# Kernel optimization log

Measured on AMD Instinct MI355X. Metric: run time of the kernel, lower is better.

The kernel has to match this reference:

```python
import math
import jax, jax.numpy as jnp
import numpy as np

V, D, E, NH, HD, L, FF, RH = 32000, 512, 4, 8, 64, 2, 2048, 256
MPL, MV = 3, 2  # max_path_len, max_visits_per_expert


def _ln(x):
    m = x.mean(-1, keepdims=True)
    v = ((x - m) ** 2).mean(-1, keepdims=True)
    return (x - m) / jnp.sqrt(v + 1e-5)


def _pe(S, d):
    pos = np.arange(S, dtype=np.float32)[:, None]
    div = np.exp(np.arange(0, d, 2, dtype=np.float32) * (-math.log(10000.0) / d))
    pe = np.zeros((S, d), np.float32)
    pe[:, 0::2] = np.sin(pos * div)
    pe[:, 1::2] = np.cos(pos * div)
    return jnp.asarray(pe)[None]  # [1,S,D]


def setup_inputs() -> dict:
    key = jax.random.key(0)
    ks = jax.random.split(key, 24)
    n = lambda k, shp, s=0.02: (jax.random.normal(k, shp, jnp.float32) * s)
    input_ids = jax.random.randint(ks[0], (8, 256), 0, V, dtype=jnp.int32)
    emb = n(ks[1], (V, D)).at[0].set(0.0)  # padding_idx=0
    return {
        "input_ids": input_ids,
        "emb": emb,
        "r_w1": n(ks[2], (RH, D)), "r_b1": jnp.zeros((RH,), jnp.float32),
        "r_w2": n(ks[3], (E + 1, RH)), "r_b2": jnp.zeros((E + 1,), jnp.float32),
        "r_q": jnp.zeros((E + 1,), jnp.float32),
        "in_w": n(ks[4], (E, L, 3 * D, D)), "in_b": jnp.zeros((E, L, 3 * D), jnp.float32),
        "out_w": n(ks[5], (E, L, D, D)), "out_b": jnp.zeros((E, L, D), jnp.float32),
        "gate_w": n(ks[6], (E, L, D, 2 * D)), "gate_b": jnp.zeros((E, L, D), jnp.float32),
        "f_w1": n(ks[7], (E, L, FF, D)), "f_b1": jnp.zeros((E, L, FF), jnp.float32),
        "f_w2": n(ks[8], (E, L, D, FF)), "f_b2": jnp.zeros((E, L, D), jnp.float32),
        "tag": n(ks[9], (E, 1, 1, D), 0.01),
        "lm_w": n(ks[10], (V, D)), "lm_b": jnp.zeros((V,), jnp.float32),
    }


def reference(input_ids, emb, r_w1, r_b1, r_w2, r_b2, r_q,
              in_w, in_b, out_w, out_b, gate_w, gate_b,
              f_w1, f_b1, f_w2, f_b2, tag, lm_w, lm_b):
    B, S = input_ids.shape

    def mha(h, w, b, ow, ob):
        qkv = h @ w.T + b  # [B,S,3D]
        q, k, v = jnp.split(qkv, 3, axis=-1)
        q = q.reshape(B, S, NH, HD); k = k.reshape(B, S, NH, HD); v = v.reshape(B, S, NH, HD)
        att = jax.nn.softmax(jnp.einsum('bqhd,bkhd->bhqk', q, k) / math.sqrt(HD), axis=-1)
        o = jnp.einsum('bhqk,bkhd->bqhd', att, v).reshape(B, S, D)
        return o @ ow.T + ob

    def expert_fwd(p, h):
        iw, ib, ow, ob, gw, gb, w1, b1, w2, b2, tg = p
        for l in range(L):
            z = _ln(h)  # norm1
            ao = mha(z, iw[l], ib[l], ow[l], ob[l])
            g = jax.nn.sigmoid(jnp.concatenate([z, ao], -1) @ gw[l].T + gb[l])
            h = h + _ln(z + g * ao)  # GatedAttention norm + residual
            z2 = _ln(h)  # norm2
            h = h + jax.nn.gelu(z2 @ w1[l].T + b1[l], approximate=False) @ w2[l].T + b2[l]
        return h + tg

    x = emb[input_ids] * math.sqrt(D)
    x = _ln(x + _pe(S, D))  # pos_encoder + input_norm (dropout=eval identity)

    visits = jnp.zeros((B, E), jnp.int32)
    active = jnp.ones((B,), bool)
    ep = (in_w, in_b, out_w, out_b, gate_w, gate_b, f_w1, f_b1, f_w2, f_b2, tag)

    for _ in range(MPL):
        summary = x.mean(axis=1)  # [B,D]
        logits = jax.nn.gelu(summary @ r_w1.T + r_b1, approximate=False) @ r_w2.T + r_b2
        fl = jnp.clip(_ln(logits + r_q[None, :]), -10.0, 10.0)
        ext = jnp.concatenate([visits >= MV, jnp.zeros((B, 1), bool)], axis=-1)
        fl = jnp.where(ext, -jnp.inf, fl)
        action = jnp.argmax(fl, axis=-1)  # E == terminate
        do = active & (action < E)
        all_out = jax.vmap(expert_fwd, in_axes=(0, None))(ep, x)  # [E,B,S,D]
        sel = jax.nn.one_hot(jnp.where(do, action, 0), E, dtype=x.dtype) * do[:, None].astype(x.dtype)
        nx = jnp.einsum('ebsd,be->bsd', all_out, sel)
        x = jnp.where(do[:, None, None], nx, x)
        visits = visits + (sel > 0).astype(jnp.int32)
        active = do

    return _ln(x) @ lm_w.T + lm_b  # final_norm + lm_head  [B,S,V]
```

## Files before the change

### kernel.cpp

```cpp
#include <hip/hip_runtime.h>
#include <hip/hip_bf16.h>
#include <math.h>

#define BB   8
#define SS   256
#define DD   512
#define NHH  8
#define HDD  64
#define EE   4
#define LL   2
#define FFF  2048
#define RHH  256
#define VV   32000
#define MVV  2
#define TOK  (BB*SS)
#define CASTBLK 44672

typedef __attribute__((ext_vector_type(8))) short bf16x8;
typedef __attribute__((ext_vector_type(4))) float f32x4;

__device__ __forceinline__ float wred_sum(float v){
#pragma unroll
  for(int o=32;o;o>>=1) v += __shfl_xor(v,o,64);
  return v;
}
__device__ __forceinline__ float block_sum(float v, float* sh){
  v = wred_sum(v);
  if((threadIdx.x&63)==0) sh[threadIdx.x>>6]=v;
  __syncthreads();
  float t = sh[0]+sh[1]+sh[2]+sh[3];
  __syncthreads();
  return t;
}
__device__ __forceinline__ float gelu_exact(float x){
  return 0.5f*x*(1.f+erff(x*0.70710678118654752f));
}
__device__ __forceinline__ unsigned short bfr(float f){
  union{float f; unsigned u;} c; c.f=f;
  unsigned u = c.u;
  return (unsigned short)((u + 0x7FFFu + ((u>>16)&1u)) >> 16);
}
__device__ __forceinline__ float bff(unsigned short u){
  union{unsigned u; float f;} c; c.u = ((unsigned)u)<<16; return c.f;
}

__global__ void k_preproc(const float* __restrict__ s0,const float* __restrict__ s1,
                          const float* __restrict__ s2,const float* __restrict__ s3,
                          const float* __restrict__ s4,const float* __restrict__ s5,
                          unsigned short* __restrict__ d0,unsigned short* __restrict__ d1,
                          unsigned short* __restrict__ d2,unsigned short* __restrict__ d3,
                          unsigned short* __restrict__ d4,unsigned short* __restrict__ d5,
                          const int* __restrict__ ids, const float* __restrict__ emb,
                          float* __restrict__ x){
  __shared__ float sh[4];
  if(blockIdx.x < CASTBLK){
    long i = (long)blockIdx.x*256 + threadIdx.x;
    const float* s; unsigned short* d; long o;
    if(i < 1572864L){ s=s0; d=d0; o=i; }
    else if(i < 2097152L){ s=s1; d=d1; o=i-1572864L; }
    else if(i < 3145728L){ s=s2; d=d2; o=i-2097152L; }
    else if(i < 5242880L){ s=s3; d=d3; o=i-3145728L; }
    else if(i < 7340032L){ s=s4; d=d4; o=i-5242880L; }
    else { s=s5; d=d5; o=i-7340032L; }
    float4 v = ((const float4*)s)[o];
    ushort4 u; u.x=bfr(v.x); u.y=bfr(v.y); u.z=bfr(v.z); u.w=bfr(v.w);
    ((ushort4*)d)[o] = u;
    return;
  }
  int tok = blockIdx.x - CASTBLK;
  int s = tok & (SS-1);
  int tid = threadIdx.x;
  int id = ids[tok];
  float v[2];
#pragma unroll
  for(int i=0;i<2;i++){
    int d = tid + i*256;
    float e = emb[(size_t)id*DD + d] * 22.627416997969522f;
    int j = d >> 1;
    float freq = expf((float)(2*j) * (-0.0179889460390160f));
    float arg = (float)s * freq;
    v[i] = e + ((d & 1) ? cosf(arg) : sinf(arg));
  }
  float m = block_sum(v[0]+v[1], sh) * (1.f/DD);
  float dd0=v[0]-m, dd1=v[1]-m;
  float var = block_sum(dd0*dd0+dd1*dd1, sh) * (1.f/DD);
  float inv = rsqrtf(var + 1e-5f);
  float* q = x + (size_t)tok*DD;
  q[tid] = dd0*inv; q[tid+256] = dd1*inv;
}

__global__ __launch_bounds__(256)
void k_compose(const unsigned short* __restrict__ out_wb, const float* __restrict__ out_b,
               const unsigned short* __restrict__ gate_wb,
               unsigned short* __restrict__ wext, float* __restrict__ cb){
  int combo = blockIdx.x;
  const unsigned short* Wa2 = gate_wb + (size_t)combo*DD*2*DD + 512;
  const unsigned short* Wo  = out_wb  + (size_t)combo*DD*DD;
  int c0 = blockIdx.y*64;
  int t = threadIdx.x;
  if(blockIdx.z == 4){
    const float* ob = out_b + (size_t)combo*DD;
    int c = c0 + (t>>2), q = t&3;
    float s = 0.f;
    for(int j=q*128; j<q*128+128; j++) s += bff(Wa2[(size_t)c*1024 + j]) * ob[j];
    s += __shfl_xor(s,1,64);
    s += __shfl_xor(s,2,64);
    if(q==0) cb[(size_t)combo*DD + c] = s;
    return;
  }
  int kb = blockIdx.z*128;
  __shared__ unsigned short sA[64*64];
  __shared__ unsigned short sWT[128*64];
  int lane = t & 63, w = t >> 6;
  int wcol0 = w*32;
  f32x4 acc[4][2];
#pragma unroll
  for(int m=0;m<4;m++)
#pragma unroll
    for(int n=0;n<2;n++) acc[m][n] = (f32x4){0.f,0.f,0.f,0.f};

  for(int j0 = 0; j0 < DD; j0 += 64){
    {
      int sr = t>>3, ss8 = t&7;
#pragma unroll
      for(int i=0;i<2;i++){
        int r = i*32 + sr;
        int ce = ((ss8<<4) ^ ((r&7)<<4)) >> 1;
        const unsigned short* gp = Wa2 + (size_t)(c0+r)*1024 + j0 + ce;
        __builtin_amdgcn_global_load_lds((const __attribute__((address_space(1))) void*)gp,
            (__attribute__((address_space(3))) void*)(sA + i*2048 + t*8), 16, 0, 0);
      }
    }
    {
      int jr = t>>2, cg = (t&3)*32;
      const unsigned short* gp = Wo + (size_t)(j0+jr)*DD + kb + cg;
      bf16x8 v0 = *(const bf16x8*)gp;
      bf16x8 v1 = *(const bf16x8*)(gp+8);
      bf16x8 v2 = *(const bf16x8*)(gp+16);
      bf16x8 v3 = *(const bf16x8*)(gp+24);
#pragma unroll
      for(int e=0;e<8;e++){
        int n0 = cg+e;
        *(unsigned short*)((char*)sWT + n0*128      + ((jr*2) ^ ((n0&7)<<4)))     = (unsigned short)v0[e];
        int n1 = cg+8+e;
        *(unsigned short*)((char*)sWT + n1*128      + ((jr*2) ^ ((n1&7)<<4)))     = (unsigned short)v1[e];
        int n2 = cg+16+e;
        *(unsigned short*)((char*)sWT + n2*128      + ((jr*2) ^ ((n2&7)<<4)))     = (unsigned short)v2[e];
        int n3 = cg+24+e;
        *(unsigned short*)((char*)sWT + n3*128      + ((jr*2) ^ ((n3&7)<<4)))     = (unsigned short)v3[e];
      }
    }
    asm volatile("s_waitcnt vmcnt(0)" ::: "memory");
    __syncthreads();
#pragma unroll
    for(int ks=0; ks<2; ks++){
      bf16x8 af[4], wf[2];
#pragma unroll
      for(int m=0;m<4;m++){
        int r = m*16 + (lane & 15);
        af[m] = *(const bf16x8*)((const char*)sA + r*128 + (((((lane>>4)<<4)|(ks<<6))) ^ ((r&7)<<4)));
      }
#pragma unroll
      for(int n=0;n<2;n++){
        int r = wcol0 + n*16 + (lane & 15);
        wf[n] = *(const bf16x8*)((const char*)sWT + r*128 + (((((lane>>4)<<4)|(ks<<6))) ^ ((r&7)<<4)));
      }
#pragma unroll
      for(int m=0;m<4;m++)
#pragma unroll
        for(int n=0;n<2;n++)
          acc[m][n] = __builtin_amdgcn_mfma_f32_16x16x32_bf16(af[m], wf[n], acc[m][n], 0, 0, 0);
    }
    __syncthreads();
  }
  int orow0 = c0 + ((lane >> 4) << 2);
  int ocol0 = kb + wcol0 + (lane & 15);
#pragma unroll
  for(int m=0;m<4;m++)
#pragma unroll
    for(int n=0;n<2;n++){
      int col = ocol0 + n*16;
#pragma unroll
      for(int j=0;j<4;j++){
        int row = orow0 + m*16 + j;
        wext[(size_t)combo*DD*DD + (size_t)row*DD + col] = bfr(acc[m][n][j]);
      }
    }
}

__global__ void k_lnpsum(const float* __restrict__ xin, const float* __restrict__ P0,
                         const float* __restrict__ P1, float* __restrict__ xout,
                         unsigned short* __restrict__ zb,
                         float* __restrict__ psum, const int* __restrict__ dof){
  __shared__ float sh[4];
  int tid = threadIdx.x;
  if(blockIdx.x < TOK){
    int tok = blockIdx.x; int b = tok>>8;
    size_t base = (size_t)tok*DD;
    float a0 = xin[base+tid], a1 = xin[base+tid+256];
    if(P0){
      if(dof[b]){
        a0 += P0[base+tid]     + P1[base+tid];
        a1 += P0[base+tid+256] + P1[base+tid+256];
      }
      xout[base+tid] = a0; xout[base+tid+256] = a1;
    }
    float m = block_sum(a0+a1, sh) * (1.f/DD);
    float d0=a0-m, d1=a1-m;
    float var = block_sum(d0*d0+d1*d1, sh) * (1.f/DD);
    float inv = rsqrtf(var + 1e-5f);
    zb[base+tid] = bfr(d0*inv); zb[base+tid+256] = bfr(d1*inv);
  } else {
    int pb = blockIdx.x - TOK; int b = pb>>4, p = pb&15;
    bool c = (P0 != nullptr) && dof[b];
    float s0=0.f, s1=0.f;
    for(int tt=0; tt<16; tt++){
      size_t r = (size_t)(b*SS + p*16 + tt)*DD;
      float v0 = xin[r+tid], v1 = xin[r+tid+256];
      if(c){ v0 += P0[r+tid]+P1[r+tid]; v1 += P0[r+tid+256]+P1[r+tid+256]; }
      s0 += v0; s1 += v1;
    }
    float* q = psum + (size_t)(b*16+p)*DD;
    q[tid] = s0; q[tid+256] = s1;
  }
}

__global__ void k_router(const float* __restrict__ psum,
                         const float* __restrict__ r_w1, const float* __restrict__ r_b1,
                         const float* __restrict__ r_w2, const float* __restrict__ r_b2,
                         const float* __restrict__ r_q,
                         int* __restrict__ action, int* __restrict__ dof,
                         int* __restrict__ visits, int* __restrict__ active, int step){
  int b = blockIdx.x; int tid = threadIdx.x;
  if(step==0 && tid==0){ active[b]=1; for(int e=0;e<EE;e++) visits[b*EE+e]=0; }
  __shared__ float ssum[DD];
  __shared__ float hid[RHH];
  __shared__ float lg[EE+1];
  float s0=0.f, s1=0.f;
  for(int p=0;p<16;p++){
    const float* q = psum + (size_t)(b*16+p)*DD;
    s0 += q[tid]; s1 += q[tid+256];
  }
  ssum[tid] = s0*(1.f/SS); ssum[tid+256] = s1*(1.f/SS);
  __syncthreads();
  float acc = r_b1[tid];
  const float4* wr4 = (const float4*)(r_w1 + (size_t)tid*DD);
  for(int d4=0; d4<DD/4; d4++){
    float4 wv = wr4[d4];
    float4 sv = *(const float4*)&ssum[d4*4];
    acc += wv.x*sv.x + wv.y*sv.y + wv.z*sv.z + wv.w*sv.w;
  }
  hid[tid] = gelu_exact(acc);
  __syncthreads();
  if(tid < EE+1){
    const float* w2 = r_w2 + (size_t)tid*RHH;
    float a = r_b2[tid] + r_q[tid];
    for(int j=0;j<RHH;j++) a += hid[j]*w2[j];
    lg[tid]=a;
  }
  __syncthreads();
  if(tid==0){
    float m=0.f; for(int k=0;k<EE+1;k++) m+=lg[k]; m *= (1.f/(EE+1));
    float v=0.f; for(int k=0;k<EE+1;k++){float d=lg[k]-m; v+=d*d;} v *= (1.f/(EE+1));
    float inv = rsqrtf(v+1e-5f);
    float best=-1e38f; int bi=0;
    for(int k=0;k<EE+1;k++){
      float fl = (lg[k]-m)*inv;
      fl = fminf(fmaxf(fl,-10.f),10.f);
      if(k<EE && visits[b*EE+k]>=MVV) fl = -1e38f;
      if(fl > best){best=fl; bi=k;}
    }
    int dd = (active[b] && bi<EE) ? 1 : 0;
    action[b]=bi; dof[b]=dd;
    if(dd) visits[b*EE+bi]++;
    active[b]=dd;
  }
}

template<int EPI>
__device__ __forceinline__ void mg64(
    unsigned short* sA, unsigned short* sW,
    const unsigned short* __restrict__ A, int Ald,
    const unsigned short* __restrict__ W, int Wld,
    const float* __restrict__ bias, const float* __restrict__ tagv,
    int N, int K,
    float* __restrict__ Cf, unsigned short* __restrict__ Cb,
    int rowbase, int colbase){
  int t = threadIdx.x;
  int lane = t & 63;
  int w = t >> 6;
  int wcol0 = w*32;
  int sr = t >> 3, ss8 = t & 7;

  f32x4 acc[4][2];
#pragma unroll
  for(int m=0;m<4;m++)
#pragma unroll
    for(int n=0;n<2;n++) acc[m][n] = (f32x4){0.f,0.f,0.f,0.f};

  auto STAGE = [&](int buf, int k0){
    unsigned short* dA = sA + buf*4096;
    unsigned short* dW = sW + buf*8192;
#pragma unroll
    for(int i = 0; i < 2; i++){
      int r  = i*32 + sr;
      int ce = ((ss8<<4) ^ ((r&7)<<4)) >> 1;
      const unsigned short* gp = A + (size_t)(rowbase + r)*Ald + k0 + ce;
      __builtin_amdgcn_global_load_lds((const __attribute__((address_space(1))) void*)gp,
          (__attribute__((address_space(3))) void*)(dA + i*2048 + t*8), 16, 0, 0);
    }
#pragma unroll
    for(int i = 0; i < 4; i++){
      int r  = i*32 + sr;
      int ce = ((ss8<<4) ^ ((r&7)<<4)) >> 1;
      const unsigned short* gw = W + (size_t)(colbase + r)*Wld + k0 + ce;
      __builtin_amdgcn_global_load_lds((const __attribute__((address_space(1))) void*)gw,
          (__attribute__((address_space(3))) void*)(dW + i*2048 + t*8), 16, 0, 0);
    }
  };

  STAGE(0, 0);
  int cur = 0;
  for(int k0 = 0; k0 < K; k0 += 64){
    if(k0 + 64 < K){
      STAGE(cur^1, k0+64);
      asm volatile("s_waitcnt vmcnt(6)" ::: "memory");
    } else {
      asm volatile("s_waitcnt vmcnt(0)" ::: "memory");
    }
    __builtin_amdgcn_s_barrier();
    __builtin_amdgcn_sched_barrier(0);
    const char* bA = (const char*)(sA + cur*4096);
    const char* bW = (const char*)(sW + cur*8192);
#pragma unroll
    for(int ks = 0; ks < 2; ks++){
      bf16x8 af[4], wf[2];
#pragma unroll
      for(int m = 0; m < 4; m++){
        int r = m*16 + (lane & 15);
        af[m] = *(const bf16x8*)(bA + r*128 + (((((lane>>4)<<4)|(ks<<6))) ^ ((r&7)<<4)));
      }
#pragma unroll
      for(int n = 0; n < 2; n++){
        int r = wcol0 + n*16 + (lane & 15);
        wf[n] = *(const bf16x8*)(bW + r*128 + (((((lane>>4)<<4)|(ks<<6))) ^ ((r&7)<<4)));
      }
#pragma unroll
      for(int m = 0; m < 4; m++)
#pragma unroll
        for(int n = 0; n < 2; n++)
          acc[m][n] = __builtin_amdgcn_mfma_f32_16x16x32_bf16(af[m], wf[n], acc[m][n], 0, 0, 0);
    }
    asm volatile("s_waitcnt lgkmcnt(0)" ::: "memory");
    __builtin_amdgcn_s_barrier();
    cur ^= 1;
  }
  int orow0 = rowbase + ((lane >> 4) << 2);
  int ocol0 = colbase + wcol0 + (lane & 15);
#pragma unroll
  for(int m = 0; m < 4; m++){
#pragma unroll
    for(int n = 0; n < 2; n++){
      int col = ocol0 + n*16;
      float addv = (bias ? bias[col] : 0.f) + (tagv ? tagv[col] : 0.f);
#pragma unroll
      for(int j = 0; j < 4; j++){
        int row = orow0 + m*16 + j;
        size_t idx = (size_t)row*N + col;
        float v = acc[m][n][j] + addv;
        if(EPI == 0){ if(Cf) Cf[idx] = v; if(Cb) Cb[idx] = bfr(v); }
        else if(EPI == 1){ Cb[idx] = bfr(gelu_exact(v)); }
        else { Cf[idx] += v; }
      }
    }
  }
}

#define GEMM_LDS __shared__ unsigned short sA[2*64*64]; __shared__ unsigned short sW[2*128*64];

__global__ __launch_bounds__(256)
void k_qkvgate(const unsigned short* __restrict__ z_bf,
               const unsigned short* __restrict__ in_wb, const float* __restrict__ in_b,
               const unsigned short* __restrict__ gate_wb, const float* __restrict__ gate_b,
               unsigned short* __restrict__ qkv_bf, float* __restrict__ gtmp, int l,
               const int* __restrict__ action, const int* __restrict__ dof){
  GEMM_LDS
  int b = blockIdx.x; if(!dof[b]) return;
  size_t o = (size_t)(action[b]*LL + l);
  int rowbase = b*SS + blockIdx.y*64;
  int zz = blockIdx.z;
  if(zz < 12){
    mg64<0>(sA,sW, z_bf,DD, in_wb + o*3*DD*DD, DD, in_b + o*3*DD, nullptr,
            3*DD, DD, nullptr, qkv_bf, rowbase, zz*128);
  } else {
    mg64<0>(sA,sW, z_bf,DD, gate_wb + o*DD*2*DD, 2*DD, gate_b + o*DD, nullptr,
            DD, DD, gtmp, nullptr, rowbase, (zz-12)*128);
  }
}

__global__ __launch_bounds__(256)
void k_outgate(const unsigned short* __restrict__ attno_bf,
               const unsigned short* __restrict__ out_wb, const float* __restrict__ out_b,
               const unsigned short* __restrict__ wext, const float* __restrict__ cb,
               unsigned short* __restrict__ ao_bf, float* __restrict__ gtmp, int l,
               const int* __restrict__ action, const int* __restrict__ dof){
  GEMM_LDS
  int b = blockIdx.x; if(!dof[b]) return;
  size_t o = (size_t)(action[b]*LL + l);
  int rowbase = b*SS + blockIdx.y*64;
  int zz = blockIdx.z;
  if(zz < 4){
    mg64<0>(sA,sW, attno_bf,DD, out_wb + o*DD*DD, DD, out_b + o*DD, nullptr,
            DD, DD, nullptr, ao_bf, rowbase, zz*128);
  } else {
    mg64<2>(sA,sW, attno_bf,DD, wext + o*DD*DD, DD, cb + o*DD, nullptr,
            DD, DD, gtmp, nullptr, rowbase, (zz-4)*128);
  }
}

__global__ __launch_bounds__(256)
void k_ffn1(const unsigned short* __restrict__ z2_bf,
            const unsigned short* __restrict__ f_w1b, const float* __restrict__ f_b1,
            unsigned short* __restrict__ ffh_bf, int l,
            const int* __restrict__ action, const int* __restrict__ dof){
  GEMM_LDS
  int b = blockIdx.x; if(!dof[b]) return;
  size_t o = (size_t)(action[b]*LL + l);
  mg64<1>(sA,sW, z2_bf,DD, f_w1b + o*FFF*DD, DD, f_b1 + o*FFF, nullptr,
          FFF, DD, nullptr, ffh_bf, b*SS + blockIdx.y*64, blockIdx.z*128);
}

__global__ __launch_bounds__(256)
void k_ffn2(const unsigned short* __restrict__ ffh_bf,
            const unsigned short* __restrict__ f_w2b, const float* __restrict__ f_b2,
            const float* __restrict__ tag,
            float* __restrict__ P0, float* __restrict__ P1, int l,
            const int* __restrict__ action, const int* __restrict__ dof){
  GEMM_LDS
  int b = blockIdx.x; if(!dof[b]) return;
  size_t o = (size_t)(action[b]*LL + l);
  int half = blockIdx.z >> 2, colb = (blockIdx.z & 3)*128;
  const float* bias = half ? nullptr : (f_b2 + o*DD);
  const float* tagv = (half==0 && l==LL-1) ? (tag + (size_t)action[b]*DD) : nullptr;
  mg64<0>(sA,sW, ffh_bf + half*1024, FFF, f_w2b + o*DD*FFF + half*1024, FFF,
          bias, tagv, DD, 1024, half ? P1 : P0, nullptr,
          b*SS + blockIdx.y*64, colb);
}

__global__ __launch_bounds__(256)
void k_attn(const unsigned short* __restrict__ qkv, unsigned short* __restrict__ attno,
            const int* __restrict__ dof){
  int bh = blockIdx.x; int b = bh>>3, h = bh&7;
  if(!dof[b]) return;
  int q0 = blockIdx.y*64;
  __shared__ unsigned short sK[256*64];
  __shared__ unsigned short sVT[64*256];
  int t = threadIdx.x, l = t&63, w = t>>6;
  const unsigned short* qbase = qkv + (size_t)b*SS*1536;

  {
    int sr = t>>3, s8 = t&7;
#pragma unroll
    for(int i=0;i<8;i++){
      int r = i*32 + sr;
      int ce = ((s8<<4) ^ ((r&7)<<4)) >> 1;
      const unsigned short* gp = qbase + (size_t)r*1536 + 512 + h*64 + ce;
      __builtin_amdgcn_global_load_lds((const __attribute__((address_space(1))) void*)gp,
          (__attribute__((address_space(3))) void*)(sK + i*2048 + t*8), 16, 0, 0);
    }
  }
  {
    int kt0 = t>>2, dg = (t&3)*16;
#pragma unroll
    for(int i=0;i<4;i++){
      int kt = i*64 + kt0;
      const unsigned short* gp = qbase + (size_t)kt*1536 + 1024 + h*64 + dg;
      bf16x8 v0 = *(const bf16x8*)gp;
      bf16x8 v1 = *(const bf16x8*)(gp+8);
#pragma unroll
      for(int e=0;e<8;e++){
        int d  = dg+e;
        *(unsigned short*)((char*)sVT + d*512  + ((kt*2) ^ ((d&7)<<4)))  = (unsigned short)v0[e];
        int d2 = dg+8+e;
        *(unsigned short*)((char*)sVT + d2*512 + ((kt*2) ^ ((d2&7)<<4))) = (unsigned short)v1[e];
      }
    }
  }
  bf16x8 qf[2];
  {
    const unsigned short* qrow = qbase + (size_t)(q0 + w*16 + (l&15))*1536 + h*64;
    qf[0] = *(const bf16x8*)(qrow + ((l>>4)<<3));
    qf[1] = *(const bf16x8*)(qrow + ((l>>4)<<3) + 32);
  }
  __syncthreads();

  f32x4 sacc[16];
#pragma unroll
  for(int kb=0;kb<16;kb++) sacc[kb] = (f32x4){0.f,0.f,0.f,0.f};
#pragma unroll
  for(int kb=0;kb<16;kb++){
    int rk = kb*16 + (l&15);
#pragma unroll
    for(int ks=0;ks<2;ks++){
      bf16x8 kf = *(const bf16x8*)((const char*)sK + rk*128 + (((((l>>4)<<4)|(ks<<6))) ^ ((rk&7)<<4)));
      sacc[kb] = __builtin_amdgcn_mfma_f32_16x16x32_bf16(qf[ks], kf, sacc[kb], 0, 0, 0);
    }
  }
  float rden[4];
#pragma unroll
  for(int j=0;j<4;j++){
    float m = -1e38f;
#pragma unroll
    for(int kb=0;kb<16;kb++) m = fmaxf(m, sacc[kb][j]);
#pragma unroll
    for(int o=1;o<16;o<<=1) m = fmaxf(m, __shfl_xor(m,o,64));
    m *= 0.125f;
    float s = 0.f;
#pragma unroll
    for(int kb=0;kb<16;kb++){
      float e = expf(sacc[kb][j]*0.125f - m);
      sacc[kb][j] = e; s += e;
    }
#pragma unroll
    for(int o=1;o<16;o<<=1) s += __shfl_xor(s,o,64);
    rden[j] = 1.f/s;
  }
  __syncthreads();

  char* sP = (char*)sK + w*8192;
#pragma unroll
  for(int kb=0;kb<16;kb++){
    int k = kb*16 + (l&15);
#pragma unroll
    for(int j=0;j<4;j++){
      int qr = ((l>>4)<<2) + j;
      *(unsigned short*)(sP + qr*512 + ((k*2) ^ ((qr&7)<<4))) = bfr(sacc[kb][j]);
    }
  }
  __syncthreads();

  f32x4 oacc[4];
#pragma unroll
  for(int df=0;df<4;df++) oacc[df] = (f32x4){0.f,0.f,0.f,0.f};
#pragma unroll
  for(int kstep=0;kstep<8;kstep++){
    bf16x8 pa = *(const bf16x8*)(sP + (l&15)*512 + ((((kstep<<6)|((l>>4)<<4))) ^ ((l&7)<<4)));
#pragma unroll
    for(int df=0;df<4;df++){
      int d = df*16 + (l&15);
      bf16x8 vb = *(const bf16x8*)((char*)sVT + d*512 + ((((kstep<<6)|((l>>4)<<4))) ^ ((d&7)<<4)));
      oacc[df] = __builtin_amdgcn_mfma_f32_16x16x32_bf16(pa, vb, oacc[df], 0, 0, 0);
    }
  }
  int orow0 = b*SS + q0 + w*16 + ((l>>4)<<2);
#pragma unroll
  for(int df=0;df<4;df++){
    int col = h*64 + df*16 + (l&15);
#pragma unroll
    for(int j=0;j<4;j++)
      attno[(size_t)(orow0+j)*DD + col] = bfr(oacc[df][j]*rden[j]);
  }
}

__global__ void k_gateres_ln(const unsigned short* __restrict__ zb,
                             const unsigned short* __restrict__ aob,
                             const float* __restrict__ g, float* __restrict__ x,
                             unsigned short* __restrict__ z2b, const int* __restrict__ dof){
  int tok = blockIdx.x; if(!dof[tok>>8]) return;
  __shared__ float sh[4];
  int tid=threadIdx.x;
  size_t base=(size_t)tok*DD;
  float zz0=bff(zb[base+tid]),     aa0=bff(aob[base+tid]),     gg0=g[base+tid];
  float zz1=bff(zb[base+tid+256]), aa1=bff(aob[base+tid+256]), gg1=g[base+tid+256];
  float t0 = zz0 + aa0/(1.f+expf(-gg0));
  float t1 = zz1 + aa1/(1.f+expf(-gg1));
  float m = block_sum(t0+t1,sh)*(1.f/DD);
  float d0=t0-m, d1=t1-m;
  float var=block_sum(d0*d0+d1*d1,sh)*(1.f/DD);
  float inv=rsqrtf(var+1e-5f);
  float xn0 = x[base+tid]     + d0*inv;
  float xn1 = x[base+tid+256] + d1*inv;
  x[base+tid] = xn0; x[base+tid+256] = xn1;
  float m2 = block_sum(xn0+xn1,sh)*(1.f/DD);
  float e0=xn0-m2, e1=xn1-m2;
  float var2=block_sum(e0*e0+e1*e1,sh)*(1.f/DD);
  float inv2=rsqrtf(var2+1e-5f);
  z2b[base+tid] = bfr(e0*inv2); z2b[base+tid+256] = bfr(e1*inv2);
}

__global__ __launch_bounds__(512)
void k_lmgemm(const unsigned short* __restrict__ A, const unsigned short* __restrict__ W,
              const float* __restrict__ bias, float* __restrict__ C){
  __shared__ unsigned short sA[2*256*64];
  __shared__ unsigned short sW[2*256*64];
  int t = threadIdx.x, lane = t & 63, w = t >> 6;
  int wr = w >> 2, wc = w & 3;
  int rowbase = blockIdx.y*256, colbase = blockIdx.z*256;
  int sr = t >> 3, ss8 = t & 7;

  f32x4 acc[8][4];
#pragma unroll
  for(int m=0;m<8;m++)
#pragma unroll
    for(int n=0;n<4;n++) acc[m][n] = (f32x4){0.f,0.f,0.f,0.f};

  auto STAGE = [&](int buf, int k0){
    unsigned short* dA = sA + buf*16384;
    unsigned short* dW = sW + buf*16384;
#pragma unroll
    for(int i = 0; i < 4; i++){
      int r  = i*64 + sr;
      int ce = ((ss8<<4) ^ ((r&7)<<4)) >> 1;
      const unsigned short* gp = A + (size_t)(rowbase + r)*DD + k0 + ce;
      __builtin_amdgcn_global_load_lds((const __attribute__((address_space(1))) void*)gp,
          (__attribute__((address_space(3))) void*)(dA + i*4096 + t*8), 16, 0, 0);
      const unsigned short* gw = W + (size_t)(colbase + r)*DD + k0 + ce;
      __builtin_amdgcn_global_load_lds((const __attribute__((address_space(1))) void*)gw,
          (__attribute__((address_space(3))) void*)(dW + i*4096 + t*8), 16, 0, 0);
    }
  };

  STAGE(0, 0);
  int cur = 0;
  for(int k0 = 0; k0 < DD; k0 += 64){
    if(k0 + 64 < DD){
      STAGE(cur^1, k0+64);
      asm volatile("s_waitcnt vmcnt(8)" ::: "memory");
    } else {
      asm volatile("s_waitcnt vmcnt(0)" ::: "memory");
    }
    __builtin_amdgcn_s_barrier();
    __builtin_amdgcn_sched_barrier(0);
    const char* bA = (const char*)(sA + cur*16384);
    const char* bW = (const char*)(sW + cur*16384);
#pragma unroll
    for(int ks = 0; ks < 2; ks++){
      bf16x8 af[8], wf[4];
#pragma unroll
      for(int m = 0; m < 8; m++){
        int r = wr*128 + m*16 + (lane & 15);
        af[m] = *(const bf16x8*)(bA + r*128 + (((((lane>>4)<<4)|(ks<<6))) ^ ((r&7)<<4)));
      }
#pragma unroll
      for(int n = 0; n < 4; n++){
        int r = wc*64 + n*16 + (lane & 15);
        wf[n] = *(const bf16x8*)(bW + r*128 + (((((lane>>4)<<4)|(ks<<6))) ^ ((r&7)<<4)));
      }
#pragma unroll
      for(int m = 0; m < 8; m++)
#pragma unroll
        for(int n = 0; n < 4; n++)
          acc[m][n] = __builtin_amdgcn_mfma_f32_16x16x32_bf16(af[m], wf[n], acc[m][n], 0, 0, 0);
    }
    asm volatile("s_waitcnt lgkmcnt(0)" ::: "memory");
    __builtin_amdgcn_s_barrier();
    cur ^= 1;
  }
  int orow0 = rowbase + wr*128 + ((lane >> 4) << 2);
  int ocol0 = colbase + wc*64 + (lane & 15);
#pragma unroll
  for(int m = 0; m < 8; m++){
#pragma unroll
    for(int n = 0; n < 4; n++){
      int col = ocol0 + n*16;
      float bv = bias[col];
#pragma unroll
      for(int j = 0; j < 4; j++){
        int row = orow0 + m*16 + j;
        C[(size_t)row*VV + col] = acc[m][n][j] + bv;
      }
    }
  }
}

extern "C" void kernel_launch(void* const* d_in, const int* in_sizes, int n_in,
                              void* d_out, int out_size, void* d_ws, size_t ws_size,
                              hipStream_t stream){
  const int*   ids   = (const int*)d_in[0];
  const float* emb   = (const float*)d_in[1];
  const float* r_w1  = (const float*)d_in[2];
  const float* r_b1  = (const float*)d_in[3];
  const float* r_w2  = (const float*)d_in[4];
  const float* r_b2  = (const float*)d_in[5];
  const float* r_q   = (const float*)d_in[6];
  const float* in_w  = (const float*)d_in[7];
  const float* in_b  = (const float*)d_in[8];
  const float* out_w = (const float*)d_in[9];
  const float* out_b = (const float*)d_in[10];
  const float* gate_w= (const float*)d_in[11];
  const float* gate_b= (const float*)d_in[12];
  const float* f_w1  = (const float*)d_in[13];
  const float* f_b1  = (const float*)d_in[14];
  const float* f_w2  = (const float*)d_in[15];
  const float* f_b2  = (const float*)d_in[16];
  const float* tag   = (const float*)d_in[17];
  const float* lm_w  = (const float*)d_in[18];
  const float* lm_b  = (const float*)d_in[19];
  float* out = (float*)d_out;
  float* ws  = (float*)d_ws;

  const size_t M = (size_t)TOK*DD;
  float* x0     = ws;
  float* x1     = ws + 1*M;
  float* gtmp   = ws + 2*M;
  float* P0     = ws + 3*M;
  float* P1     = ws + 4*M;
  float* psum   = ws + 5*M;
  float* cbias  = ws + 5*M + 65536;
  int*   ipool  = (int*)(ws + 5*M + 65536 + 4096);
  int* action = ipool; int* dof = ipool+BB; int* active = ipool+2*BB; int* visits = ipool+3*BB;

  unsigned short* ub = (unsigned short*)(ws + 5*M + 65536 + 4096 + 64);
  unsigned short* z_bf     = ub;
  unsigned short* z2_bf    = ub + 1*M;
  unsigned short* attno_bf = ub + 2*M;
  unsigned short* ao_bf    = ub + 3*M;
  unsigned short* qkv_bf   = ub + 4*M;
  unsigned short* ffh_bf   = ub + 7*M;
  unsigned short* wb = ub + 11*M;
  unsigned short* in_wb   = wb;
  unsigned short* out_wb  = in_wb  + (size_t)EE*LL*3*DD*DD;
  unsigned short* gate_wb = out_wb + (size_t)EE*LL*DD*DD;
  unsigned short* f_w1b   = gate_wb+ (size_t)EE*LL*DD*2*DD;
  unsigned short* f_w2b   = f_w1b  + (size_t)EE*LL*FFF*DD;
  unsigned short* lm_wb   = f_w2b  + (size_t)EE*LL*DD*FFF;
  unsigned short* wext_b  = lm_wb  + (size_t)VV*DD;

  k_preproc<<<CASTBLK+TOK,256,0,stream>>>(in_w,out_w,gate_w,f_w1,f_w2,lm_w,
                                          in_wb,out_wb,gate_wb,f_w1b,f_w2b,lm_wb,
                                          ids, emb, x0);
  k_compose<<<dim3(8,8,5),256,0,stream>>>(out_wb, out_b, gate_wb, wext_b, cbias);

  float* xc = x0;
  for(int step=0; step<3; step++){
    float* xn = (xc==x0) ? x1 : x0;
    if(step==0)
      k_lnpsum<<<TOK+128,256,0,stream>>>(xc, nullptr, nullptr, xn, z_bf, psum, dof);
    else{
      k_lnpsum<<<TOK+128,256,0,stream>>>(xc, P0, P1, xn, z_bf, psum, dof);
      xc = xn;
    }
    k_router<<<BB,256,0,stream>>>(psum,r_w1,r_b1,r_w2,r_b2,r_q,action,dof,visits,active,step);
    for(int l=0; l<LL; l++){
      if(l==1){
        float* xn2 = (xc==x0) ? x1 : x0;
        k_lnpsum<<<TOK,256,0,stream>>>(xc, P0, P1, xn2, z_bf, nullptr, dof);
        xc = xn2;
      }
      k_qkvgate<<<dim3(BB,4,16),256,0,stream>>>(z_bf, in_wb,in_b, gate_wb,gate_b,
                                                qkv_bf, gtmp, l, action, dof);
      k_attn<<<dim3(BB*NHH,4),256,0,stream>>>(qkv_bf, attno_bf, dof);
      k_outgate<<<dim3(BB,4,8),256,0,stream>>>(attno_bf, out_wb,out_b, wext_b,cbias,
                                               ao_bf, gtmp, l, action, dof);
      k_gateres_ln<<<TOK,256,0,stream>>>(z_bf, ao_bf, gtmp, xc, z2_bf, dof);
      k_ffn1<<<dim3(BB,4,16),256,0,stream>>>(z2_bf, f_w1b,f_b1, ffh_bf, l, action, dof);
      k_ffn2<<<dim3(BB,4,8),256,0,stream>>>(ffh_bf, f_w2b,f_b2, tag, P0, P1, l, action, dof);
    }
  }

  {
    float* xn = (xc==x0) ? x1 : x0;
    k_lnpsum<<<TOK,256,0,stream>>>(xc, P0, P1, xn, z_bf, nullptr, dof);
  }
  k_lmgemm<<<dim3(1,8,VV/256),512,0,stream>>>(z_bf, lm_wb, lm_b, out);
}
```

Measured before the change: 730.7 us.

## Fuse per-layer kernels into one persistent kernel with grid barriers

Replaces the six per-layer launches (qkv/gate GEMM, attention, out/gate GEMM, gated residual LN, FFN1, FFN2) with a single 256-block persistent kernel. The stages are separated by a software grid-wide barrier built on atomics, and work units are mapped onto fixed blocks. This removes kernel launch gaps and idle tails between small stages. The cost is reduced parallelism for the stages that previously used 512 blocks, a 64KB static LDS allocation that may limit occupancy, and reliance on all 256 blocks being co-resident for the spin barrier to avoid deadlock.

```diff
diff --git a/kernel.cpp b/kernel.cpp
--- a/kernel.cpp
+++ b/kernel.cpp
@@ -44,6 +44,24 @@
   union{unsigned u; float f;} c; c.u = ((unsigned)u)<<16; return c.f;
 }
 
+__device__ __forceinline__ void gsync(unsigned* cnt, unsigned* gen){
+  __syncthreads();
+  if(threadIdx.x==0){
+    __threadfence();
+    unsigned g = __hip_atomic_load(gen, __ATOMIC_RELAXED, __HIP_MEMORY_SCOPE_AGENT);
+    unsigned a = __hip_atomic_fetch_add(cnt, 1u, __ATOMIC_ACQ_REL, __HIP_MEMORY_SCOPE_AGENT);
+    if(a == 255u){
+      __hip_atomic_store(cnt, 0u, __ATOMIC_RELAXED, __HIP_MEMORY_SCOPE_AGENT);
+      __hip_atomic_store(gen, g+1u, __ATOMIC_RELEASE, __HIP_MEMORY_SCOPE_AGENT);
+    } else {
+      while(__hip_atomic_load(gen, __ATOMIC_RELAXED, __HIP_MEMORY_SCOPE_AGENT) == g)
+        __builtin_amdgcn_s_sleep(4);
+    }
+    __threadfence();
+  }
+  __syncthreads();
+}
+
 __global__ void k_preproc(const float* __restrict__ s0,const float* __restrict__ s1,
                           const float* __restrict__ s2,const float* __restrict__ s3,
                           const float* __restrict__ s4,const float* __restrict__ s5,
@@ -51,8 +69,9 @@
                           unsigned short* __restrict__ d2,unsigned short* __restrict__ d3,
                           unsigned short* __restrict__ d4,unsigned short* __restrict__ d5,
                           const int* __restrict__ ids, const float* __restrict__ emb,
-                          float* __restrict__ x){
+                          float* __restrict__ x, unsigned* bcnt, unsigned* bgen){
   __shared__ float sh[4];
+  if(blockIdx.x==0 && threadIdx.x==0){ *bcnt = 0u; *bgen = 0u; }
   if(blockIdx.x < CASTBLK){
     long i = (long)blockIdx.x*256 + threadIdx.x;
     const float* s; unsigned short* d; long o;
@@ -141,13 +160,13 @@
 #pragma unroll
       for(int e=0;e<8;e++){
         int n0 = cg+e;
-        *(unsigned short*)((char*)sWT + n0*128      + ((jr*2) ^ ((n0&7)<<4)))     = (unsigned short)v0[e];
+        *(unsigned short*)((char*)sWT + n0*128 + ((jr*2) ^ ((n0&7)<<4))) = (unsigned short)v0[e];
         int n1 = cg+8+e;
-        *(unsigned short*)((char*)sWT + n1*128      + ((jr*2) ^ ((n1&7)<<4)))     = (unsigned short)v1[e];
+        *(unsigned short*)((char*)sWT + n1*128 + ((jr*2) ^ ((n1&7)<<4))) = (unsigned short)v1[e];
         int n2 = cg+16+e;
-        *(unsigned short*)((char*)sWT + n2*128      + ((jr*2) ^ ((n2&7)<<4)))     = (unsigned short)v2[e];
+        *(unsigned short*)((char*)sWT + n2*128 + ((jr*2) ^ ((n2&7)<<4))) = (unsigned short)v2[e];
         int n3 = cg+24+e;
-        *(unsigned short*)((char*)sWT + n3*128      + ((jr*2) ^ ((n3&7)<<4)))     = (unsigned short)v3[e];
+        *(unsigned short*)((char*)sWT + n3*128 + ((jr*2) ^ ((n3&7)<<4))) = (unsigned short)v3[e];
       }
     }
     asm volatile("s_waitcnt vmcnt(0)" ::: "memory");
@@ -376,86 +395,70 @@
   }
 }
 
-#define GEMM_LDS __shared__ unsigned short sA[2*64*64]; __shared__ unsigned short sW[2*128*64];
-
-__global__ __launch_bounds__(256)
-void k_qkvgate(const unsigned short* __restrict__ z_bf,
-               const unsigned short* __restrict__ in_wb, const float* __restrict__ in_b,
-               const unsigned short* __restrict__ gate_wb, const float* __restrict__ gate_b,
-               unsigned short* __restrict__ qkv_bf, float* __restrict__ gtmp, int l,
-               const int* __restrict__ action, const int* __restrict__ dof){
-  GEMM_LDS
-  int b = blockIdx.x; if(!dof[b]) return;
+__device__ __forceinline__ void qkvgate_unit(char* smem, const unsigned short* z_bf,
+    const unsigned short* in_wb, const float* in_b,
+    const unsigned short* gate_wb, const float* gate_b,
+    unsigned short* qkv_bf, float* gtmp, int l, const int* action,
+    int b, int y, int z){
+  unsigned short* sA = (unsigned short*)smem;
+  unsigned short* sW = (unsigned short*)(smem + 16384);
   size_t o = (size_t)(action[b]*LL + l);
-  int rowbase = b*SS + blockIdx.y*64;
-  int zz = blockIdx.z;
-  if(zz < 12){
+  int rowbase = b*SS + y*64;
+  if(z < 12)
     mg64<0>(sA,sW, z_bf,DD, in_wb + o*3*DD*DD, DD, in_b + o*3*DD, nullptr,
-            3*DD, DD, nullptr, qkv_bf, rowbase, zz*128);
-  } else {
+            3*DD, DD, nullptr, qkv_bf, rowbase, z*128);
+  else
     mg64<0>(sA,sW, z_bf,DD, gate_wb + o*DD*2*DD, 2*DD, gate_b + o*DD, nullptr,
-            DD, DD, gtmp, nullptr, rowbase, (zz-12)*128);
-  }
-}
-
-__global__ __launch_bounds__(256)
-void k_outgate(const unsigned short* __restrict__ attno_bf,
-               const unsigned short* __restrict__ out_wb, const float* __restrict__ out_b,
-               const unsigned short* __restrict__ wext, const float* __restrict__ cb,
-               unsigned short* __restrict__ ao_bf, float* __restrict__ gtmp, int l,
-               const int* __restrict__ action, const int* __restrict__ dof){
-  GEMM_LDS
-  int b = blockIdx.x; if(!dof[b]) return;
+            DD, DD, gtmp, nullptr, rowbase, (z-12)*128);
+}
+
+__device__ __forceinline__ void outgate_unit(char* smem, const unsigned short* attno_bf,
+    const unsigned short* out_wb, const float* out_b,
+    const unsigned short* wext, const float* cb,
+    unsigned short* ao_bf, float* gtmp, int l, const int* action,
+    int b, int y, int z){
+  unsigned short* sA = (unsigned short*)smem;
+  unsigned short* sW = (unsigned short*)(smem + 16384);
   size_t o = (size_t)(action[b]*LL + l);
-  int rowbase = b*SS + blockIdx.y*64;
-  int zz = blockIdx.z;
-  if(zz < 4){
+  int rowbase = b*SS + y*64;
+  if(z < 4)
     mg64<0>(sA,sW, attno_bf,DD, out_wb + o*DD*DD, DD, out_b + o*DD, nullptr,
-            DD, DD, nullptr, ao_bf, rowbase, zz*128);
-  } else {
+            DD, DD, nullptr, ao_bf, rowbase, z*128);
+  else
     mg64<2>(sA,sW, attno_bf,DD, wext + o*DD*DD, DD, cb + o*DD, nullptr,
-            DD, DD, gtmp, nullptr, rowbase, (zz-4)*128);
-  }
-}
-
-__global__ __launch_bounds__(256)
-void k_ffn1(const unsigned short* __restrict__ z2_bf,
-            const unsigned short* __restrict__ f_w1b, const float* __restrict__ f_b1,
-            unsigned short* __restrict__ ffh_bf, int l,
-            const int* __restrict__ action, const int* __restrict__ dof){
-  GEMM_LDS
-  int b = blockIdx.x; if(!dof[b]) return;
+            DD, DD, gtmp, nullptr, rowbase, (z-4)*128);
+}
+
+__device__ __forceinline__ void ffn1_unit(char* smem, const unsigned short* z2_bf,
+    const unsigned short* f_w1b, const float* f_b1,
+    unsigned short* ffh_bf, int l, const int* action, int b, int y, int z){
+  unsigned short* sA = (unsigned short*)smem;
+  unsigned short* sW = (unsigned short*)(smem + 16384);
   size_t o = (size_t)(action[b]*LL + l);
   mg64<1>(sA,sW, z2_bf,DD, f_w1b + o*FFF*DD, DD, f_b1 + o*FFF, nullptr,
-          FFF, DD, nullptr, ffh_bf, b*SS + blockIdx.y*64, blockIdx.z*128);
-}
-
-__global__ __launch_bounds__(256)
-void k_ffn2(const unsigned short* __restrict__ ffh_bf,
-            const unsigned short* __restrict__ f_w2b, const float* __restrict__ f_b2,
-            const float* __restrict__ tag,
-            float* __restrict__ P0, float* __restrict__ P1, int l,
-            const int* __restrict__ action, const int* __restrict__ dof){
-  GEMM_LDS
-  int b = blockIdx.x; if(!dof[b]) return;
+          FFF, DD, nullptr, ffh_bf, b*SS + y*64, z*128);
+}
+
+__device__ __forceinline__ void ffn2_unit(char* smem, const unsigned short* ffh_bf,
+    const unsigned short* f_w2b, const float* f_b2, const float* tag,
+    float* P0, float* P1, int l, const int* action, int b, int y, int z){
+  unsigned short* sA = (unsigned short*)smem;
+  unsigned short* sW = (unsigned short*)(smem + 16384);
   size_t o = (size_t)(action[b]*LL + l);
-  int half = blockIdx.z >> 2, colb = (blockIdx.z & 3)*128;
+  int half = z >> 2, colb = (z & 3)*128;
   const float* bias = half ? nullptr : (f_b2 + o*DD);
   const float* tagv = (half==0 && l==LL-1) ? (tag + (size_t)action[b]*DD) : nullptr;
   mg64<0>(sA,sW, ffh_bf + half*1024, FFF, f_w2b + o*DD*FFF + half*1024, FFF,
           bias, tagv, DD, 1024, half ? P1 : P0, nullptr,
-          b*SS + blockIdx.y*64, colb);
-}
-
-__global__ __launch_bounds__(256)
-void k_attn(const unsigned short* __restrict__ qkv, unsigned short* __restrict__ attno,
-            const int* __restrict__ dof){
-  int bh = blockIdx.x; int b = bh>>3, h = bh&7;
-  if(!dof[b]) return;
-  int q0 = blockIdx.y*64;
-  __shared__ unsigned short sK[256*64];
-  __shared__ unsigned short sVT[64*256];
-  int t = threadIdx.x, l = t&63, w = t>>6;
+          b*SS + y*64, colb);
+}
+
+__device__ __forceinline__ void attn_unit(char* smem,
+    const unsigned short* __restrict__ qkv, unsigned short* __restrict__ attno,
+    int b, int h, int q0){
+  unsigned short* sK  = (unsigned short*)smem;
+  unsigned short* sVT = (unsigned short*)(smem + 32768);
+  int t = threadIdx.x, ln = t&63, w = t>>6;
   const unsigned short* qbase = qkv + (size_t)b*SS*1536;
 
   {
@@ -488,9 +491,9 @@
   }
   bf16x8 qf[2];
   {
-    const unsigned short* qrow = qbase + (size_t)(q0 + w*16 + (l&15))*1536 + h*64;
-    qf[0] = *(const bf16x8*)(qrow + ((l>>4)<<3));
-    qf[1] = *(const bf16x8*)(qrow + ((l>>4)<<3) + 32);
+    const unsigned short* qrow = qbase + (size_t)(q0 + w*16 + (ln&15))*1536 + h*64;
+    qf[0] = *(const bf16x8*)(qrow + ((ln>>4)<<3));
+    qf[1] = *(const bf16x8*)(qrow + ((ln>>4)<<3) + 32);
   }
   __syncthreads();
 
@@ -499,10 +502,10 @@
   for(int kb=0;kb<16;kb++) sacc[kb] = (f32x4){0.f,0.f,0.f,0.f};
 #pragma unroll
   for(int kb=0;kb<16;kb++){
-    int rk = kb*16 + (l&15);
+    int rk = kb*16 + (ln&15);
 #pragma unroll
     for(int ks=0;ks<2;ks++){
-      bf16x8 kf = *(const bf16x8*)((const char*)sK + rk*128 + (((((l>>4)<<4)|(ks<<6))) ^ ((rk&7)<<4)));
+      bf16x8 kf = *(const bf16x8*)((const char*)sK + rk*128 + (((((ln>>4)<<4)|(ks<<6))) ^ ((rk&7)<<4)));
       sacc[kb] = __builtin_amdgcn_mfma_f32_16x16x32_bf16(qf[ks], kf, sacc[kb], 0, 0, 0);
     }
   }
@@ -530,10 +533,10 @@
   char* sP = (char*)sK + w*8192;
 #pragma unroll
   for(int kb=0;kb<16;kb++){
-    int k = kb*16 + (l&15);
+    int k = kb*16 + (ln&15);
 #pragma unroll
     for(int j=0;j<4;j++){
-      int qr = ((l>>4)<<2) + j;
+      int qr = ((ln>>4)<<2) + j;
       *(unsigned short*)(sP + qr*512 + ((k*2) ^ ((qr&7)<<4))) = bfr(sacc[kb][j]);
     }
   }
@@ -544,30 +547,29 @@
   for(int df=0;df<4;df++) oacc[df] = (f32x4){0.f,0.f,0.f,0.f};
 #pragma unroll
   for(int kstep=0;kstep<8;kstep++){
-    bf16x8 pa = *(const bf16x8*)(sP + (l&15)*512 + ((((kstep<<6)|((l>>4)<<4))) ^ ((l&7)<<4)));
+    bf16x8 pa = *(const bf16x8*)(sP + (ln&15)*512 + ((((kstep<<6)|((ln>>4)<<4))) ^ ((ln&7)<<4)));
 #pragma unroll
     for(int df=0;df<4;df++){
-      int d = df*16 + (l&15);
-      bf16x8 vb = *(const bf16x8*)((char*)sVT + d*512 + ((((kstep<<6)|((l>>4)<<4))) ^ ((d&7)<<4)));
+      int d = df*16 + (ln&15);
+      bf16x8 vb = *(const bf16x8*)((char*)sVT + d*512 + ((((kstep<<6)|((ln>>4)<<4))) ^ ((d&7)<<4)));
       oacc[df] = __builtin_amdgcn_mfma_f32_16x16x32_bf16(pa, vb, oacc[df], 0, 0, 0);
     }
   }
-  int orow0 = b*SS + q0 + w*16 + ((l>>4)<<2);
+  int orow0 = b*SS + q0 + w*16 + ((ln>>4)<<2);
 #pragma unroll
   for(int df=0;df<4;df++){
-    int col = h*64 + df*16 + (l&15);
+    int col = h*64 + df*16 + (ln&15);
 #pragma unroll
     for(int j=0;j<4;j++)
       attno[(size_t)(orow0+j)*DD + col] = bfr(oacc[df][j]*rden[j]);
   }
 }
 
-__global__ void k_gateres_ln(const unsigned short* __restrict__ zb,
-                             const unsigned short* __restrict__ aob,
-                             const float* __restrict__ g, float* __restrict__ x,
-                             unsigned short* __restrict__ z2b, const int* __restrict__ dof){
-  int tok = blockIdx.x; if(!dof[tok>>8]) return;
-  __shared__ float sh[4];
+__device__ __forceinline__ void gateres_unit(char* smem,
+    const unsigned short* __restrict__ zb, const unsigned short* __restrict__ aob,
+    const float* __restrict__ g, float* __restrict__ x,
+    unsigned short* __restrict__ z2b, int tok){
+  float* sh = (float*)smem;
   int tid=threadIdx.x;
   size_t base=(size_t)tok*DD;
   float zz0=bff(zb[base+tid]),     aa0=bff(aob[base+tid]),     gg0=g[base+tid];
@@ -586,6 +588,64 @@
   float var2=block_sum(e0*e0+e1*e1,sh)*(1.f/DD);
   float inv2=rsqrtf(var2+1e-5f);
   z2b[base+tid] = bfr(e0*inv2); z2b[base+tid+256] = bfr(e1*inv2);
+}
+
+__global__ __launch_bounds__(256)
+void k_layer(const unsigned short* __restrict__ z_bf,
+             const unsigned short* __restrict__ in_wb, const float* __restrict__ in_b,
+             const unsigned short* __restrict__ gate_wb, const float* __restrict__ gate_b,
+             unsigned short* __restrict__ qkv_bf, float* __restrict__ gtmp,
+             unsigned short* __restrict__ attno_bf,
+             const unsigned short* __restrict__ out_wb, const float* __restrict__ out_b,
+             const unsigned short* __restrict__ wext, const float* __restrict__ cb,
+             unsigned short* __restrict__ ao_bf,
+             float* __restrict__ x, unsigned short* __restrict__ z2_bf,
+             const unsigned short* __restrict__ f_w1b, const float* __restrict__ f_b1,
+             unsigned short* __restrict__ ffh_bf,
+             const unsigned short* __restrict__ f_w2b, const float* __restrict__ f_b2,
+             const float* __restrict__ tag,
+             float* __restrict__ P0, float* __restrict__ P1, int l,
+             const int* __restrict__ action, const int* __restrict__ dof,
+             unsigned* bcnt, unsigned* bgen){
+  __shared__ char smem[65536];
+  int bx = blockIdx.x;
+  int b = bx & 7;
+  int e = bx >> 3;
+  bool act = dof[b] != 0;
+
+  if(act){
+#pragma unroll
+    for(int i=0;i<2;i++){
+      int u = e + i*32;
+      qkvgate_unit(smem, z_bf, in_wb, in_b, gate_wb, gate_b, qkv_bf, gtmp, l, action,
+                   b, u & 3, u >> 2);
+    }
+  }
+  gsync(bcnt,bgen);
+
+  if(act) attn_unit(smem, qkv_bf, attno_bf, b, e & 7, (e >> 3) * 64);
+  gsync(bcnt,bgen);
+
+  if(act) outgate_unit(smem, attno_bf, out_wb, out_b, wext, cb, ao_bf, gtmp, l, action,
+                       b, e & 3, e >> 2);
+  gsync(bcnt,bgen);
+
+  if(act){
+    for(int i=0;i<8;i++)
+      gateres_unit(smem, z_bf, ao_bf, gtmp, x, z2_bf, b*SS + e + i*32);
+  }
+  gsync(bcnt,bgen);
+
+  if(act){
+#pragma unroll
+    for(int i=0;i<2;i++){
+      int u = e + i*32;
+      ffn1_unit(smem, z2_bf, f_w1b, f_b1, ffh_bf, l, action, b, u & 3, u >> 2);
+    }
+  }
+  gsync(bcnt,bgen);
+
+  if(act) ffn2_unit(smem, ffh_bf, f_w2b, f_b2, tag, P0, P1, l, action, b, e & 3, e >> 2);
 }
 
 __global__ __launch_bounds__(512)
@@ -709,6 +769,8 @@
   float* cbias  = ws + 5*M + 65536;
   int*   ipool  = (int*)(ws + 5*M + 65536 + 4096);
   int* action = ipool; int* dof = ipool+BB; int* active = ipool+2*BB; int* visits = ipool+3*BB;
+  unsigned* bcnt = (unsigned*)(ipool + 32);
+  unsigned* bgen = (unsigned*)(ipool + 48);
 
   unsigned short* ub = (unsigned short*)(ws + 5*M + 65536 + 4096 + 64);
   unsigned short* z_bf     = ub;
@@ -728,7 +790,7 @@
 
   k_preproc<<<CASTBLK+TOK,256,0,stream>>>(in_w,out_w,gate_w,f_w1,f_w2,lm_w,
                                           in_wb,out_wb,gate_wb,f_w1b,f_w2b,lm_wb,
-                                          ids, emb, x0);
+                                          ids, emb, x0, bcnt, bgen);
   k_compose<<<dim3(8,8,5),256,0,stream>>>(out_wb, out_b, gate_wb, wext_b, cbias);
 
   float* xc = x0;
@@ -747,14 +809,10 @@
         k_lnpsum<<<TOK,256,0,stream>>>(xc, P0, P1, xn2, z_bf, nullptr, dof);
         xc = xn2;
       }
-      k_qkvgate<<<dim3(BB,4,16),256,0,stream>>>(z_bf, in_wb,in_b, gate_wb,gate_b,
-                                                qkv_bf, gtmp, l, action, dof);
-      k_attn<<<dim3(BB*NHH,4),256,0,stream>>>(qkv_bf, attno_bf, dof);
-      k_outgate<<<dim3(BB,4,8),256,0,stream>>>(attno_bf, out_wb,out_b, wext_b,cbias,
-                                               ao_bf, gtmp, l, action, dof);
-      k_gateres_ln<<<TOK,256,0,stream>>>(z_bf, ao_bf, gtmp, xc, z2_bf, dof);
-      k_ffn1<<<dim3(BB,4,16),256,0,stream>>>(z2_bf, f_w1b,f_b1, ffh_bf, l, action, dof);
-      k_ffn2<<<dim3(BB,4,8),256,0,stream>>>(ffh_bf, f_w2b,f_b2, tag, P0, P1, l, action, dof);
+      k_layer<<<256,256,0,stream>>>(z_bf, in_wb,in_b, gate_wb,gate_b, qkv_bf, gtmp,
+                                    attno_bf, out_wb,out_b, wext_b,cbias, ao_bf,
+                                    xc, z2_bf, f_w1b,f_b1, ffh_bf, f_w2b,f_b2, tag,
+                                    P0, P1, l, action, dof, bcnt, bgen);
     }
   }
 
```

Result: slower. 1.588 ms (+117.3%).
